# Optimization experiments

Hardware: AMD Instinct MI355X
Metric: run time of the kernel (lower is better)

## Reference

```python
import jax, jax.numpy as jnp
import numpy as np

ENCODER_DIM, HIDDEN_DIM, ATT_DIM = 2048, 1024, 1024
B, P = 128, 196  # batch, num_pixels


def setup_inputs() -> dict:
    key = jax.random.key(0)
    ks = jax.random.split(key, 8)
    s_e = 1.0 / np.sqrt(ENCODER_DIM)
    s_h = 1.0 / np.sqrt(HIDDEN_DIM)
    s_a = 1.0 / np.sqrt(ATT_DIM)
    return {
        "encoder_out": jax.random.normal(ks[0], (B, P, ENCODER_DIM), jnp.float32),
        "decoder_hidden": jax.random.normal(ks[1], (B, HIDDEN_DIM), jnp.float32),
        # nn.Linear params (weight is [out, in] in torch; store transposed for x @ W)
        "W_enc": jax.random.uniform(ks[2], (ENCODER_DIM, ATT_DIM), jnp.float32, -s_e, s_e),
        "b_enc": jax.random.uniform(ks[3], (ATT_DIM,), jnp.float32, -s_e, s_e),
        "W_dec": jax.random.uniform(ks[4], (HIDDEN_DIM, ATT_DIM), jnp.float32, -s_h, s_h),
        "b_dec": jax.random.uniform(ks[5], (ATT_DIM,), jnp.float32, -s_h, s_h),
        "W_full": jax.random.uniform(ks[6], (ATT_DIM,), jnp.float32, -s_a, s_a),
        "b_full": jax.random.uniform(ks[7], (), jnp.float32, -s_a, s_a),
    }


def reference(encoder_out, decoder_hidden, W_enc, b_enc, W_dec, b_dec, W_full, b_full):
    # att1: [B, P, A]; att2: [B, 1, A]
    att1 = jnp.einsum("bpe,ea->bpa", encoder_out, W_enc) + b_enc
    att2 = decoder_hidden @ W_dec + b_dec
    att = jax.nn.relu(att1 + att2[:, None, :])
    scores = jnp.einsum("bpa,a->bp", att, W_full) + b_full  # [B, P]
    alpha = jax.nn.softmax(scores, axis=1)
    context = jnp.einsum("bpe,bp->be", encoder_out, alpha)  # [B, E]
    return (context, alpha)
```

## Files before the change

kernel.cpp:

```cpp
#include <hip/hip_runtime.h>
#include <hip/hip_bf16.h>


#define B_   128
#define P_   196
#define E_   2048
#define H_   1024
#define A_   1024
#define M_   (B_ * P_)
#define NKSTEP (E_ / 64)

typedef __bf16 bf16x8 __attribute__((ext_vector_type(8)));
typedef float f32x4 __attribute__((ext_vector_type(4)));

__device__ __bf16 g_wt[(size_t)A_ * E_];
__device__ __bf16 g_enc[(size_t)M_ * E_];

__device__ __forceinline__ bf16x8 cvt8r(const float4 a, const float4 b) {
    bf16x8 r;
    r[0] = (__bf16)a.x; r[1] = (__bf16)a.y; r[2] = (__bf16)a.z; r[3] = (__bf16)a.w;
    r[4] = (__bf16)b.x; r[5] = (__bf16)b.y; r[6] = (__bf16)b.z; r[7] = (__bf16)b.w;
    return r;
}

__device__ __forceinline__ void gl16(const void* g, void* l) {
    __builtin_amdgcn_global_load_lds(
        (const __attribute__((address_space(1))) unsigned int*)g,
        (__attribute__((address_space(3))) unsigned int*)l, 16, 0, 0);
}

__global__ __launch_bounds__(256) void k_pre(
    const float* __restrict__ enc, const float* __restrict__ w,
    const float* __restrict__ dh, const float* __restrict__ wdec,
    const float* __restrict__ benc, const float* __restrict__ bdec,
    float* __restrict__ scores, float* __restrict__ att2p) {
    __shared__ float smem[10240];
    const int bid = blockIdx.x;
    const int t = threadIdx.x;

    if (bid < 1792) {
        size_t i = ((size_t)bid * 256 + t) * 8;
        const size_t stride = (size_t)1792 * 256 * 8;
#pragma unroll
        for (int it = 0; it < 14; ++it, i += stride) {
            const float4 a = *(const float4*)(enc + i);
            const float4 b = *(const float4*)(enc + i + 4);
            *(bf16x8*)&g_enc[i] = cvt8r(a, b);
        }
    } else if (bid < 1920) {
        __bf16* tile = (__bf16*)smem;
        const int er = t >> 2, c0 = (t & 3) * 16;
        const int ar = t >> 2, es0 = (t & 3) * 16;
#pragma unroll 1
        for (int j = 0; j < 4; ++j) {
            const int job = (bid - 1792) * 4 + j;
            const int a0 = (job & 15) * 64, e0 = (job >> 4) * 64;
            __syncthreads();
#pragma unroll
            for (int jj = 0; jj < 4; ++jj) {
                const float4 v = *(const float4*)&w[(size_t)(e0 + er) * A_ +
                                                    a0 + c0 + jj * 4];
                tile[(c0 + jj * 4 + 0) * 72 + er] = (__bf16)v.x;
                tile[(c0 + jj * 4 + 1) * 72 + er] = (__bf16)v.y;
                tile[(c0 + jj * 4 + 2) * 72 + er] = (__bf16)v.z;
                tile[(c0 + jj * 4 + 3) * 72 + er] = (__bf16)v.w;
            }
            __syncthreads();
            *(bf16x8*)&g_wt[(size_t)(a0 + ar) * E_ + e0 + es0] =
                *(const bf16x8*)&tile[ar * 72 + es0];
            *(bf16x8*)&g_wt[(size_t)(a0 + ar) * E_ + e0 + es0 + 8] =
                *(const bf16x8*)&tile[ar * 72 + es0 + 8];
        }
    } else {
        const int vbid = bid - 1920;
        const int a0 = (vbid & 7) * 128;
        const int b0 = (vbid >> 3) * 8;
        const int gi = vbid * 256 + t;
        if (gi < M_) scores[gi] = 0.f;
        float (*hs)[H_] = (float (*)[H_])smem;
        float (*red)[8] = (float (*)[8])(smem + 8192);
        for (int i = t; i < 8 * H_; i += 256)
            hs[i >> 10][i & 1023] =
                dh[(size_t)(b0 + (i >> 10)) * H_ + (i & 1023)];
        __syncthreads();
        const int a = a0 + (t & 127);
        const int h0 = (t >> 7) * 512;
        float acc[8] = {};
#pragma unroll 4
        for (int h = 0; h < 512; ++h) {
            const float wv = wdec[(size_t)(h0 + h) * A_ + a];
#pragma unroll
            for (int j = 0; j < 8; ++j) acc[j] += hs[j][h0 + h] * wv;
        }
#pragma unroll
        for (int j = 0; j < 8; ++j) red[t][j] = acc[j];
        __syncthreads();
        if (t < 128) {
            const float bb = benc[a0 + t] + bdec[a0 + t];
#pragma unroll
            for (int j = 0; j < 8; ++j)
                att2p[(size_t)(b0 + j) * A_ + a0 + t] =
                    red[t][j] + red[t + 128][j] + bb;
        }
    }
}

__global__ __launch_bounds__(256, 2) void k_gemm_scores(
    const float* __restrict__ att2p,
    const float* __restrict__ wfull,
    float* __restrict__ scores) {
    __shared__ __align__(16) __bf16 As[2][128 * 64];
    __shared__ __align__(16) __bf16 Bs[2][128 * 64];
    __shared__ float red[2][128];

    const int t = threadIdx.x;
    const int lane = t & 63;
    const int wave = t >> 6;
    const int wm = wave >> 1, wn = wave & 1;
    const int q = lane >> 4, r = lane & 15;
    const int orig = blockIdx.y * 8 + blockIdx.x;
    const int L = (orig & 7) * (M_ / 128) + (orig >> 3);
    const int bn = L & 7, bm = L >> 3;
    const int m0 = bm * 128, n0 = bn * 128;

    const int rbase = wave * 8 + (lane >> 3);
    const int cx = ((t & 7) ^ ((t >> 3) & 7)) * 16;
    const char* pa = (const char*)g_enc + (size_t)(m0 + rbase) * 4096 + cx;
    const char* pb = (const char*)g_wt  + (size_t)(n0 + rbase) * 4096 + cx;
    char* ad0 = (char*)&As[0][0] + wave * 1024;
    char* ad1 = (char*)&As[1][0] + wave * 1024;
    char* bd0 = (char*)&Bs[0][0] + wave * 1024;
    char* bd1 = (char*)&Bs[1][0] + wave * 1024;

    f32x4 acc[4][4] = {};

#pragma unroll
    for (int i = 0; i < 4; ++i)
        gl16(pa + (size_t)i * 131072, ad0 + i * 4096);
#pragma unroll
    for (int i = 0; i < 4; ++i)
        gl16(pb + (size_t)i * 131072, bd0 + i * 4096);

    int cur = 0;
    for (int kt = 0; kt < NKSTEP; ++kt) {
        asm volatile("s_waitcnt vmcnt(0)" ::: "memory");
        asm volatile("s_waitcnt lgkmcnt(0)" ::: "memory");
        __builtin_amdgcn_s_barrier();

        const char* AsC = (const char*)&As[cur][0];
        const char* BsC = (const char*)&Bs[cur][0];

        if (kt + 1 < NKSTEP) {
            char* ad = cur ? ad0 : ad1;
            char* bd = cur ? bd0 : bd1;
            const size_t ko = (size_t)(kt + 1) * 128;
#pragma unroll
            for (int i = 0; i < 4; ++i)
                gl16(pa + (size_t)i * 131072 + ko, ad + i * 4096);
#pragma unroll
            for (int i = 0; i < 4; ++i)
                gl16(pb + (size_t)i * 131072 + ko, bd + i * 4096);
        }

#pragma unroll
        for (int ks = 0; ks < 2; ++ks) {
            bf16x8 af[4], bfv[4];
#pragma unroll
            for (int f = 0; f < 4; ++f) {
                const int mf = wm * 64 + f * 16 + r;
                af[f] = *(const bf16x8*)(AsC + mf * 128 +
                        ((ks * 64 + q * 16) ^ ((r & 7) << 4)));
            }
#pragma unroll
            for (int f = 0; f < 4; ++f) {
                const int nf = wn * 64 + f * 16 + r;
                bfv[f] = *(const bf16x8*)(BsC + nf * 128 +
                        ((ks * 64 + q * 16) ^ ((r & 7) << 4)));
            }
#pragma unroll
            for (int fm = 0; fm < 4; ++fm)
#pragma unroll
                for (int fn = 0; fn < 4; ++fn)
                    acc[fm][fn] = __builtin_amdgcn_mfma_f32_16x16x32_bf16(
                        af[fm], bfv[fn], acc[fm][fn], 0, 0, 0);
        }
        cur ^= 1;
    }

    float psum[4][4];
    const float* wfb = wfull + n0 + wn * 64;
#pragma unroll
    for (int fm = 0; fm < 4; ++fm) {
#pragma unroll
        for (int i = 0; i < 4; ++i) {
            const int row_g = m0 + wm * 64 + fm * 16 + q * 4 + i;
            const unsigned bidx = (unsigned)row_g / 196u;
            const float* a2 = att2p + (size_t)bidx * A_ + n0 + wn * 64;
            float s = 0.f;
#pragma unroll
            for (int fn = 0; fn < 4; ++fn) {
                const int cl = fn * 16 + r;
                float v = acc[fm][fn][i] + a2[cl];
                v = fmaxf(v, 0.f);
                s += v * wfb[cl];
            }
            psum[fm][i] = s;
        }
    }
#pragma unroll
    for (int fm = 0; fm < 4; ++fm)
#pragma unroll
        for (int i = 0; i < 4; ++i) {
            float v = psum[fm][i];
            v += __shfl_xor(v, 1);
            v += __shfl_xor(v, 2);
            v += __shfl_xor(v, 4);
            v += __shfl_xor(v, 8);
            if (r == 0) red[wn][wm * 64 + fm * 16 + q * 4 + i] = v;
        }
    __syncthreads();
    if (t < 128) atomicAdd(&scores[m0 + t], red[0][t] + red[1][t]);
}

__global__ __launch_bounds__(256) void k_softmax(
    const float* __restrict__ scores, float* __restrict__ out) {
    const int b = blockIdx.x;
    const int t = threadIdx.x;
    __shared__ float sm[256];
    const bool act = t < P_;
    const float val = act ? scores[b * P_ + t] : 0.f;
    sm[t] = act ? val : -1e30f;
    __syncthreads();
    for (int off = 128; off > 0; off >>= 1) {
        if (t < off) sm[t] = fmaxf(sm[t], sm[t + off]);
        __syncthreads();
    }
    const float mx = sm[0];
    __syncthreads();
    const float e = act ? __expf(val - mx) : 0.f;
    sm[t] = e;
    __syncthreads();
    for (int off = 128; off > 0; off >>= 1) {
        if (t < off) sm[t] = sm[t] + sm[t + off];
        __syncthreads();
    }
    const float inv = 1.0f / sm[0];
    if (act) out[(size_t)B_ * E_ + b * P_ + t] = e * inv;
}

__global__ __launch_bounds__(256) void k_context(float* __restrict__ out) {
    const int b = blockIdx.y;
    const int e0 = blockIdx.x * 512 + threadIdx.x * 2;
    __shared__ float al[P_];
    if (threadIdx.x < P_)
        al[threadIdx.x] = out[(size_t)B_ * E_ + b * P_ + threadIdx.x];
    __syncthreads();
    float ax = 0.f, ay = 0.f;
    const char* base = (const char*)g_enc +
                       ((size_t)b * P_) * (E_ * 2) + (size_t)e0 * 2;
#pragma unroll 14
    for (int p = 0; p < P_; ++p) {
        const unsigned u = *(const unsigned*)(base + (size_t)p * (E_ * 2));
        const float ap = al[p];
        ax += ap * __uint_as_float(u << 16);
        ay += ap * __uint_as_float(u & 0xffff0000u);
    }
    float2 sv; sv.x = ax; sv.y = ay;
    *(float2*)(out + (size_t)b * E_ + e0) = sv;
}

extern "C" void kernel_launch(void* const* d_in, const int* in_sizes, int n_in,
                              void* d_out, int out_size, void* d_ws,
                              size_t ws_size, hipStream_t stream) {
    const float* enc   = (const float*)d_in[0];
    const float* dh    = (const float*)d_in[1];
    const float* wenc  = (const float*)d_in[2];
    const float* benc  = (const float*)d_in[3];
    const float* wdec  = (const float*)d_in[4];
    const float* bdec  = (const float*)d_in[5];
    const float* wfull = (const float*)d_in[6];
    float* out = (float*)d_out;

    float* att2p  = out;
    float* scores = (float*)((char*)d_out + 524288);

    k_pre<<<2048, 256, 0, stream>>>(enc, wenc, dh, wdec, benc, bdec, scores,
                                    att2p);
    k_gemm_scores<<<dim3(8, M_ / 128), 256, 0, stream>>>(att2p, wfull,
                                                         scores);
    k_softmax<<<B_, 256, 0, stream>>>(scores, out);
    k_context<<<dim3(4, 128), 256, 0, stream>>>(out);
}
```

Measured before the change: 567.0 us.

## Restructure scores GEMM into 256x256 tiles with 8-wave ping-pong pipeline

Rewrites the fused GEMM+score kernel to use 256x256 output tiles with 512 threads (8 waves, 2x4 layout), splitting each K step into quarter-tile sub-phases. Shared-memory reads, async global-to-LDS stages and MFMA blocks are interleaved with barriers and s_setprio so that loads overlap compute. Larger tiles cut global traffic per FLOP, and the grid becomes a flat 392-block launch with a remapped block order. The cost is higher register pressure (8x4 accumulators), occupancy of one block per CU, and intricate manual waitcnt bookkeeping.

```diff
diff --git a/kernel.cpp b/kernel.cpp
--- a/kernel.cpp
+++ b/kernel.cpp
@@ -105,121 +105,154 @@
     }
 }
 
-__global__ __launch_bounds__(256, 2) void k_gemm_scores(
+__global__ __launch_bounds__(512, 1) void k_gemm_scores(
     const float* __restrict__ att2p,
     const float* __restrict__ wfull,
     float* __restrict__ scores) {
-    __shared__ __align__(16) __bf16 As[2][128 * 64];
-    __shared__ __align__(16) __bf16 Bs[2][128 * 64];
-    __shared__ float red[2][128];
+    __shared__ __align__(16) __bf16 As[2][2][2][64][64];
+    __shared__ __align__(16) __bf16 Bs[2][2][4][32][64];
 
     const int t = threadIdx.x;
-    const int lane = t & 63;
-    const int wave = t >> 6;
-    const int wm = wave >> 1, wn = wave & 1;
+    const int lane = t & 63, w = t >> 6;
+    const int wm = w >> 2, wn = w & 3;
     const int q = lane >> 4, r = lane & 15;
-    const int orig = blockIdx.y * 8 + blockIdx.x;
-    const int L = (orig & 7) * (M_ / 128) + (orig >> 3);
-    const int bn = L & 7, bm = L >> 3;
-    const int m0 = bm * 128, n0 = bn * 128;
-
-    const int rbase = wave * 8 + (lane >> 3);
-    const int cx = ((t & 7) ^ ((t >> 3) & 7)) * 16;
-    const char* pa = (const char*)g_enc + (size_t)(m0 + rbase) * 4096 + cx;
-    const char* pb = (const char*)g_wt  + (size_t)(n0 + rbase) * 4096 + cx;
-    char* ad0 = (char*)&As[0][0] + wave * 1024;
-    char* ad1 = (char*)&As[1][0] + wave * 1024;
-    char* bd0 = (char*)&Bs[0][0] + wave * 1024;
-    char* bd1 = (char*)&Bs[1][0] + wave * 1024;
-
-    f32x4 acc[4][4] = {};
-
-#pragma unroll
-    for (int i = 0; i < 4; ++i)
-        gl16(pa + (size_t)i * 131072, ad0 + i * 4096);
-#pragma unroll
-    for (int i = 0; i < 4; ++i)
-        gl16(pb + (size_t)i * 131072, bd0 + i * 4096);
-
-    int cur = 0;
-    for (int kt = 0; kt < NKSTEP; ++kt) {
-        asm volatile("s_waitcnt vmcnt(0)" ::: "memory");
-        asm volatile("s_waitcnt lgkmcnt(0)" ::: "memory");
-        __builtin_amdgcn_s_barrier();
-
-        const char* AsC = (const char*)&As[cur][0];
-        const char* BsC = (const char*)&Bs[cur][0];
-
-        if (kt + 1 < NKSTEP) {
-            char* ad = cur ? ad0 : ad1;
-            char* bd = cur ? bd0 : bd1;
-            const size_t ko = (size_t)(kt + 1) * 128;
-#pragma unroll
-            for (int i = 0; i < 4; ++i)
-                gl16(pa + (size_t)i * 131072 + ko, ad + i * 4096);
-#pragma unroll
-            for (int i = 0; i < 4; ++i)
-                gl16(pb + (size_t)i * 131072 + ko, bd + i * 4096);
-        }
-
-#pragma unroll
-        for (int ks = 0; ks < 2; ++ks) {
-            bf16x8 af[4], bfv[4];
-#pragma unroll
-            for (int f = 0; f < 4; ++f) {
-                const int mf = wm * 64 + f * 16 + r;
-                af[f] = *(const bf16x8*)(AsC + mf * 128 +
-                        ((ks * 64 + q * 16) ^ ((r & 7) << 4)));
-            }
-#pragma unroll
-            for (int f = 0; f < 4; ++f) {
-                const int nf = wn * 64 + f * 16 + r;
-                bfv[f] = *(const bf16x8*)(BsC + nf * 128 +
-                        ((ks * 64 + q * 16) ^ ((r & 7) << 4)));
-            }
-#pragma unroll
-            for (int fm = 0; fm < 4; ++fm)
-#pragma unroll
-                for (int fn = 0; fn < 4; ++fn)
-                    acc[fm][fn] = __builtin_amdgcn_mfma_f32_16x16x32_bf16(
-                        af[fm], bfv[fn], acc[fm][fn], 0, 0, 0);
-        }
-        cur ^= 1;
-    }
-
-    float psum[4][4];
+    const int orig = blockIdx.x;
+    const int L = (orig & 7) * 49 + (orig >> 3);
+    const int bn = L & 3, bm = L >> 2;
+    const int m0 = bm * 256, n0 = bn * 256;
+
+    const int swz = ((t & 7) ^ ((t >> 3) & 7)) * 16;
+    const char* gA = (const char*)g_enc + (size_t)(m0 + (t >> 3)) * 4096 + swz;
+    const char* gB = (const char*)g_wt +
+        (size_t)(n0 + (t >> 8) * 64 + ((t >> 3) & 31)) * 4096 + swz;
+
+    const int kx0 = (q * 16) ^ ((r & 7) << 4);
+    const int kx1 = (64 + q * 16) ^ ((r & 7) << 4);
+
+    bf16x8 af[4][2], bf0[2][2], bf1[2][2];
+    f32x4 acc[8][4] = {};
+
+#define STG_A(slot, h, kt) do { \
+    gl16(gA + ((size_t)(h) * 64) * 4096 + (size_t)(kt) * 128, \
+         (char*)As + (slot) * 32768 + (h) * 16384 + w * 1024); \
+    gl16(gA + ((size_t)(h) * 64 + 128) * 4096 + (size_t)(kt) * 128, \
+         (char*)As + (slot) * 32768 + (h) * 16384 + 8192 + w * 1024); } while (0)
+#define STG_B(slot, h, kt) do { \
+    gl16(gB + ((size_t)(h) * 32) * 4096 + (size_t)(kt) * 128, \
+         (char*)Bs + (slot) * 32768 + (h) * 16384 + w * 1024); \
+    gl16(gB + ((size_t)(h) * 32 + 128) * 4096 + (size_t)(kt) * 128, \
+         (char*)Bs + (slot) * 32768 + (h) * 16384 + 8192 + w * 1024); } while (0)
+
+#define RD_A(slot, mh) do { \
+    _Pragma("unroll") \
+    for (int fl = 0; fl < 4; ++fl) { \
+        const char* p_ = (const char*)As + (slot) * 32768 + (mh) * 16384 + \
+                         wm * 8192 + (fl * 16 + r) * 128; \
+        af[fl][0] = *(const bf16x8*)(p_ + kx0); \
+        af[fl][1] = *(const bf16x8*)(p_ + kx1); } } while (0)
+#define RD_B(slot, nh, B) do { \
+    _Pragma("unroll") \
+    for (int nl = 0; nl < 2; ++nl) { \
+        const char* p_ = (const char*)Bs + (slot) * 32768 + (nh) * 16384 + \
+                         wn * 4096 + (nl * 16 + r) * 128; \
+        B[nl][0] = *(const bf16x8*)(p_ + kx0); \
+        B[nl][1] = *(const bf16x8*)(p_ + kx1); } } while (0)
+#define MM16(MH, NH, B) do { \
+    _Pragma("unroll") \
+    for (int fl = 0; fl < 4; ++fl) { \
+        _Pragma("unroll") \
+        for (int nl = 0; nl < 2; ++nl) { \
+            acc[(MH)*4+fl][(NH)*2+nl] = __builtin_amdgcn_mfma_f32_16x16x32_bf16( \
+                af[fl][0], B[nl][0], acc[(MH)*4+fl][(NH)*2+nl], 0, 0, 0); \
+            acc[(MH)*4+fl][(NH)*2+nl] = __builtin_amdgcn_mfma_f32_16x16x32_bf16( \
+                af[fl][1], B[nl][1], acc[(MH)*4+fl][(NH)*2+nl], 0, 0, 0); } } } while (0)
+#define BAR() do { __builtin_amdgcn_sched_barrier(0); \
+                   __builtin_amdgcn_s_barrier(); } while (0)
+#define PRIO_MM(MH, NH, B) do { __builtin_amdgcn_s_setprio(1); \
+    MM16(MH, NH, B); __builtin_amdgcn_s_setprio(0); } while (0)
+
+    STG_A(0, 0, 0); STG_B(0, 0, 0); STG_A(0, 1, 0); STG_B(0, 1, 0);
+    STG_A(1, 0, 1); STG_B(1, 0, 1);
+    asm volatile("s_waitcnt vmcnt(4)" ::: "memory");
+    BAR();
+
+    for (int i = 0; i < 15; ++i) {
+        const int kb = 2 * i + 1, ka2 = 2 * i + 2, kb2 = 2 * i + 3;
+        RD_A(0, 0); RD_B(0, 0, bf0); STG_A(1, 1, kb); BAR();
+        PRIO_MM(0, 0, bf0); BAR();
+        RD_B(0, 1, bf1); STG_B(1, 1, kb); BAR();
+        PRIO_MM(0, 1, bf1); BAR();
+        RD_A(0, 1); STG_A(0, 0, ka2); BAR();
+        PRIO_MM(1, 0, bf0); BAR();
+        STG_B(0, 0, ka2);
+        asm volatile("s_waitcnt vmcnt(4)" ::: "memory");
+        BAR();
+        PRIO_MM(1, 1, bf1); BAR();
+        RD_A(1, 0); RD_B(1, 0, bf0); STG_A(0, 1, ka2); BAR();
+        PRIO_MM(0, 0, bf0); BAR();
+        RD_B(1, 1, bf1); STG_B(0, 1, ka2); BAR();
+        PRIO_MM(0, 1, bf1); BAR();
+        RD_A(1, 1); STG_A(1, 0, kb2); BAR();
+        PRIO_MM(1, 0, bf0); BAR();
+        STG_B(1, 0, kb2);
+        asm volatile("s_waitcnt vmcnt(4)" ::: "memory");
+        BAR();
+        PRIO_MM(1, 1, bf1); BAR();
+    }
+    RD_A(0, 0); RD_B(0, 0, bf0); STG_A(1, 1, 31); BAR();
+    PRIO_MM(0, 0, bf0); BAR();
+    RD_B(0, 1, bf1); STG_B(1, 1, 31); BAR();
+    PRIO_MM(0, 1, bf1); BAR();
+    RD_A(0, 1); BAR();
+    PRIO_MM(1, 0, bf0); BAR();
+    asm volatile("s_waitcnt vmcnt(0)" ::: "memory");
+    BAR();
+    PRIO_MM(1, 1, bf1); BAR();
+    RD_A(1, 0); RD_B(1, 0, bf0); BAR();
+    PRIO_MM(0, 0, bf0); BAR();
+    RD_B(1, 1, bf1); BAR();
+    PRIO_MM(0, 1, bf1); BAR();
+    RD_A(1, 1); BAR();
+    PRIO_MM(1, 0, bf0); BAR();
+    BAR();
+    PRIO_MM(1, 1, bf1); BAR();
+
+    float* red = (float*)As;
     const float* wfb = wfull + n0 + wn * 64;
 #pragma unroll
-    for (int fm = 0; fm < 4; ++fm) {
-#pragma unroll
-        for (int i = 0; i < 4; ++i) {
-            const int row_g = m0 + wm * 64 + fm * 16 + q * 4 + i;
+    for (int f = 0; f < 8; ++f) {
+#pragma unroll
+        for (int i2 = 0; i2 < 4; ++i2) {
+            const int row256 = wm * 128 + f * 16 + q * 4 + i2;
+            const int row_g = m0 + row256;
             const unsigned bidx = (unsigned)row_g / 196u;
             const float* a2 = att2p + (size_t)bidx * A_ + n0 + wn * 64;
             float s = 0.f;
 #pragma unroll
             for (int fn = 0; fn < 4; ++fn) {
                 const int cl = fn * 16 + r;
-                float v = acc[fm][fn][i] + a2[cl];
+                float v = acc[f][fn][i2] + a2[cl];
                 v = fmaxf(v, 0.f);
                 s += v * wfb[cl];
             }
-            psum[fm][i] = s;
-        }
-    }
-#pragma unroll
-    for (int fm = 0; fm < 4; ++fm)
-#pragma unroll
-        for (int i = 0; i < 4; ++i) {
-            float v = psum[fm][i];
-            v += __shfl_xor(v, 1);
-            v += __shfl_xor(v, 2);
-            v += __shfl_xor(v, 4);
-            v += __shfl_xor(v, 8);
-            if (r == 0) red[wn][wm * 64 + fm * 16 + q * 4 + i] = v;
-        }
-    __syncthreads();
-    if (t < 128) atomicAdd(&scores[m0 + t], red[0][t] + red[1][t]);
+            s += __shfl_xor(s, 1);
+            s += __shfl_xor(s, 2);
+            s += __shfl_xor(s, 4);
+            s += __shfl_xor(s, 8);
+            if (r == 0) red[row256 * 4 + wn] = s;
+        }
+    }
+    __syncthreads();
+    if (t < 256)
+        atomicAdd(&scores[m0 + t],
+                  red[t * 4] + red[t * 4 + 1] + red[t * 4 + 2] + red[t * 4 + 3]);
+#undef STG_A
+#undef STG_B
+#undef RD_A
+#undef RD_B
+#undef MM16
+#undef BAR
+#undef PRIO_MM
 }
 
 __global__ __launch_bounds__(256) void k_softmax(
@@ -286,8 +319,7 @@
 
     k_pre<<<2048, 256, 0, stream>>>(enc, wenc, dh, wdec, benc, bdec, scores,
                                     att2p);
-    k_gemm_scores<<<dim3(8, M_ / 128), 256, 0, stream>>>(att2p, wfull,
-                                                         scores);
+    k_gemm_scores<<<392, 512, 0, stream>>>(att2p, wfull, scores);
     k_softmax<<<B_, 256, 0, stream>>>(scores, out);
-    k_context<<<dim3(4, 128), 256, 0, stream>>>(out);
-}
+    k_context<<<dim3(4, B_), 256, 0, stream>>>(out);
+}
```

Result: faster. 527.8 us (-6.9%).
